# Kernel tuning notes

Measured on AMD Instinct MI355X. Metric: run time of the kernel, lower is better.

## Reference

```python
import jax, jax.numpy as jnp
import numpy as np

H = 16       # num_heads
D = 128      # head dim (TokenShift requires D in {16,32,64,128})
BASE = 10000.0


def _shift_linear(x, W, Ws):
    # ShiftLinear: linear -> (B,T,H,D), then token_shift mixing current token
    # with previous token using data-dependent per-head weights.
    B, T, _ = x.shape
    y = (x @ W.T).reshape(B, T, H, D)
    p = jax.nn.sigmoid(x @ Ws.T)                      # (B,T,H) prev-token weight
    y_prev = jnp.pad(y, ((0, 0), (1, 0), (0, 0), (0, 0)))[:, :T]  # shift right by 1
    return y * (1.0 - p)[..., None] + y_prev * p[..., None]


def _rope(q, k):
    # Non-interleaved half-rotation, signs exactly as in the torch source:
    # y1 = x1*cos + x2*sin ; y2 = -x1*sin + x2*cos
    T = q.shape[1]
    half = D // 2
    inv = 1.0 / (BASE ** (jnp.arange(0, D, 2, dtype=jnp.float32) / D))  # (half,)
    freqs = jnp.outer(jnp.arange(T, dtype=jnp.float32), inv)            # (T,half)
    cos = jnp.cos(freqs)[None, :, None, :]
    sin = jnp.sin(freqs)[None, :, None, :]
    def rot(x):
        x1, x2 = x[..., :half], x[..., half:]
        return jnp.concatenate([x1 * cos + x2 * sin, -x1 * sin + x2 * cos], axis=-1)
    return rot(q), rot(k)


def setup_inputs() -> dict:
    key = jax.random.key(0)
    ks = jax.random.split(key, 10)
    B, T, C = 2, 2048, 2048
    s = 0.02
    return {
        "x":   jax.random.normal(ks[0], (B, T, C), jnp.float32),
        "Wq":  s * jax.random.normal(ks[1], (C, C), jnp.float32),
        "Wsq": s * jax.random.normal(ks[2], (H, C), jnp.float32),
        "Wk":  s * jax.random.normal(ks[3], (C, C), jnp.float32),
        "Wsk": s * jax.random.normal(ks[4], (H, C), jnp.float32),
        "Wv":  s * jax.random.normal(ks[5], (C, C), jnp.float32),
        "Wsv": s * jax.random.normal(ks[6], (H, C), jnp.float32),
        "Wf":  s * jax.random.normal(ks[7], (H, C), jnp.float32),
        "bf":  s * jax.random.normal(ks[8], (H,), jnp.float32),
        "Wo":  s * jax.random.normal(ks[9], (C, C), jnp.float32),
    }


def reference(x, Wq, Wsq, Wk, Wsk, Wv, Wsv, Wf, bf, Wo):
    B, T, C = x.shape
    q = _shift_linear(x, Wq, Wsq)          # (B,T,H,D)
    k = _shift_linear(x, Wk, Wsk)
    v = _shift_linear(x, Wv, Wsv)
    q, k = _rope(q, k)

    # forget gate: log f_t per head, cumulative log-decay
    logf = jax.nn.log_sigmoid(x @ Wf.T + bf)       # (B,T,H)
    cum = jnp.cumsum(logf, axis=1).transpose(0, 2, 1)  # (B,H,T)

    s = jnp.einsum('bthd,bshd->bhts', q, k) / np.sqrt(D).astype(np.float32)
    # decay bias D_ij = sum_{l=j+1}^{i} log f_l = cum_i - cum_j
    s = s + cum[:, :, :, None] - cum[:, :, None, :]
    causal = jnp.tril(jnp.ones((T, T), dtype=bool))
    s = jnp.where(causal[None, None], s, -jnp.inf)
    p = jax.nn.softmax(s, axis=-1)                 # (B,H,T,T)

    o = jnp.einsum('bhts,bshd->bthd', p, v).reshape(B, T, C)
    return o @ Wo.T
```

## Files before the change

### kernel.cpp

```cpp
#include <hip/hip_runtime.h>
#include <math.h>


typedef __attribute__((ext_vector_type(8))) short  shortx8;
typedef __attribute__((ext_vector_type(4))) float  floatx4;

#define DEV __device__ __forceinline__

DEV unsigned short f2bf(float f) {
    unsigned int u = __builtin_bit_cast(unsigned int, f);
    u += 0x7FFFu + ((u >> 16) & 1u);
    return (unsigned short)(u >> 16);
}
DEV float bf2f(unsigned short s) {
    unsigned int u = ((unsigned int)s) << 16;
    return __builtin_bit_cast(float, u);
}
DEV void async16(void* lds, const void* g) {
    __builtin_amdgcn_global_load_lds(
        (const __attribute__((address_space(1))) unsigned int*)g,
        (__attribute__((address_space(3))) unsigned int*)lds, 16, 0, 0);
}

__global__ void cvt_bf16(const float* __restrict__ in, unsigned short* __restrict__ out, int n8) {
    int i = blockIdx.x * 256 + threadIdx.x;
    if (i >= n8) return;
    float4 u = ((const float4*)in)[2 * i];
    float4 v = ((const float4*)in)[2 * i + 1];
    shortx8 r;
    r[0] = (short)f2bf(u.x); r[1] = (short)f2bf(u.y); r[2] = (short)f2bf(u.z); r[3] = (short)f2bf(u.w);
    r[4] = (short)f2bf(v.x); r[5] = (short)f2bf(v.y); r[6] = (short)f2bf(v.z); r[7] = (short)f2bf(v.w);
    *(shortx8*)(out + (size_t)i * 8) = r;
}

__global__ void build_wcat(const float* __restrict__ Wsq, const float* __restrict__ Wsk,
                           const float* __restrict__ Wsv, const float* __restrict__ Wf,
                           unsigned short* __restrict__ out) {
    int i = blockIdx.x * 256 + threadIdx.x;
    int c8 = i & 255;
    int row = i >> 8;
    const float* src = nullptr;
    if      (row < 16) src = Wsq + (size_t)row * 2048;
    else if (row < 32) src = Wsk + (size_t)(row - 16) * 2048;
    else if (row < 48) src = Wsv + (size_t)(row - 32) * 2048;
    else if (row < 64) src = Wf  + (size_t)(row - 48) * 2048;
    shortx8 r = (shortx8){0,0,0,0,0,0,0,0};
    if (src) {
#pragma unroll
        for (int q = 0; q < 8; ++q) r[q] = (short)f2bf(src[c8 * 8 + q]);
    }
    *(shortx8*)(out + (size_t)i * 8) = r;
}

template <typename OutT>
__global__ __launch_bounds__(256)
void gemm_bt(const unsigned short* __restrict__ A, const unsigned short* __restrict__ B,
             OutT* __restrict__ C, int M, int N, int K) {
    __shared__ __align__(16) unsigned short As[2][128 * 32];
    __shared__ __align__(16) unsigned short Bs[2][128 * 32];
    const int tid  = threadIdx.x;
    const int lane = tid & 63;
    const int w    = tid >> 6;
    const int m0   = blockIdx.x * 128;
    const int n0   = blockIdx.y * 128;
    const int wr   = (w >> 1) * 64;
    const int wc   = (w & 1) * 64;
    const int l15  = lane & 15, lg = lane >> 4;
    const int nk   = K >> 5;
    const int c0   = w * 64 + lane;

    floatx4 acc[4][4];
#pragma unroll
    for (int i = 0; i < 4; ++i)
#pragma unroll
        for (int j = 0; j < 4; ++j) acc[i][j] = (floatx4){0.f, 0.f, 0.f, 0.f};

#pragma unroll
    for (int t = 0; t < 2; ++t) {
        int c = t * 256 + c0;
        int row = c >> 2, seg = c & 3;
        async16(&As[0][(t * 256 + w * 64) * 8], A + (size_t)(m0 + row) * K + seg * 8);
        async16(&Bs[0][(t * 256 + w * 64) * 8], B + (size_t)(n0 + row) * K + seg * 8);
    }
    int cur = 0;
    for (int kt = 0; kt < nk; ++kt) {
        __syncthreads();
        if (kt + 1 < nk) {
#pragma unroll
            for (int t = 0; t < 2; ++t) {
                int c = t * 256 + c0;
                int row = c >> 2, seg = c & 3;
                async16(&As[cur ^ 1][(t * 256 + w * 64) * 8],
                        A + (size_t)(m0 + row) * K + (kt + 1) * 32 + seg * 8);
                async16(&Bs[cur ^ 1][(t * 256 + w * 64) * 8],
                        B + (size_t)(n0 + row) * K + (kt + 1) * 32 + seg * 8);
            }
        }
        shortx8 af[4], bfr[4];
#pragma unroll
        for (int i = 0; i < 4; ++i) {
            af[i]  = *(const shortx8*)&As[cur][(wr + i * 16 + l15) * 32 + 8 * lg];
            bfr[i] = *(const shortx8*)&Bs[cur][(wc + i * 16 + l15) * 32 + 8 * lg];
        }
#pragma unroll
        for (int i = 0; i < 4; ++i)
#pragma unroll
            for (int j = 0; j < 4; ++j)
                acc[i][j] = __builtin_amdgcn_mfma_f32_16x16x32_bf16(af[i], bfr[j], acc[i][j], 0, 0, 0);
        cur ^= 1;
    }
#pragma unroll
    for (int i = 0; i < 4; ++i)
#pragma unroll
        for (int j = 0; j < 4; ++j)
#pragma unroll
            for (int r = 0; r < 4; ++r) {
                int row = m0 + wr + i * 16 + 4 * lg + r;
                int col = n0 + wc + j * 16 + l15;
                float v = acc[i][j][r];
                if constexpr (sizeof(OutT) == 2) C[(size_t)row * N + col] = (OutT)f2bf(v);
                else                             C[(size_t)row * N + col] = v;
            }
}

__global__ void cumsum_logf(const float* __restrict__ glog, const float* __restrict__ bfv,
                            float* __restrict__ cum) {
    __shared__ float sums[256];
    const int bh = blockIdx.x, b = bh >> 4, h = bh & 15;
    const int tid = threadIdx.x;
    const float bias = bfv[h];
    float v[8];
    float s = 0.f;
#pragma unroll
    for (int i = 0; i < 8; ++i) {
        int t = tid * 8 + i;
        float z = glog[(size_t)(b * 2048 + t) * 128 + 48 + h] + bias;
        float lf = (z >= 0.f) ? -log1pf(__expf(-z)) : (z - log1pf(__expf(z)));
        s += lf;
        v[i] = s;
    }
    sums[tid] = s;
    __syncthreads();
    for (int off = 1; off < 256; off <<= 1) {
        float t = (tid >= off) ? sums[tid - off] : 0.f;
        __syncthreads();
        sums[tid] += t;
        __syncthreads();
    }
    float basep = sums[tid] - s;
#pragma unroll
    for (int i = 0; i < 8; ++i)
        cum[(size_t)bh * 2048 + tid * 8 + i] = basep + v[i];
}

template <bool ROPE>
__global__ void shift_rope(const unsigned short* __restrict__ Y, int ldY, int yoff,
                           const float* __restrict__ glog, int gcol,
                           unsigned short* __restrict__ Out) {
    int gid = blockIdx.x * 256 + threadIdx.x;
    int j = gid & 7;
    int h = (gid >> 3) & 15;
    int t = (gid >> 7) & 2047;
    int b = gid >> 18;
    const unsigned short* yp = Y + (size_t)(b * 2048 + t) * ldY + yoff + h * 128;
    float z  = glog[(size_t)(b * 2048 + t) * 128 + gcol + h];
    float pg = 1.f / (1.f + __expf(-z));
    shortx8 a1 = *(const shortx8*)(yp + j * 8);
    shortx8 a2 = *(const shortx8*)(yp + 64 + j * 8);
    shortx8 b1 = (shortx8){0,0,0,0,0,0,0,0}, b2 = b1;
    if (t > 0) {
        b1 = *(const shortx8*)(yp - ldY + j * 8);
        b2 = *(const shortx8*)(yp - ldY + 64 + j * 8);
    }
    shortx8 o1, o2;
    const float kf = 13.287712379549449f / 64.f;
#pragma unroll
    for (int i = 0; i < 8; ++i) {
        float m1 = bf2f((unsigned short)a1[i]) * (1.f - pg) + bf2f((unsigned short)b1[i]) * pg;
        float m2 = bf2f((unsigned short)a2[i]) * (1.f - pg) + bf2f((unsigned short)b2[i]) * pg;
        float r1, r2;
        if (ROPE) {
            int d = j * 8 + i;
            float inv = exp2f(-(float)d * kf);
            float ang = (float)t * inv;
            float sv, cv;
            sincosf(ang, &sv, &cv);
            r1 =  m1 * cv + m2 * sv;
            r2 = -m1 * sv + m2 * cv;
        } else { r1 = m1; r2 = m2; }
        o1[i] = (short)f2bf(r1);
        o2[i] = (short)f2bf(r2);
    }
    unsigned short* op = Out + (size_t)((b * 16 + h) * 2048 + t) * 128;
    *(shortx8*)(op + j * 8)      = o1;
    *(shortx8*)(op + 64 + j * 8) = o2;
}

__global__ void transpose_v(const unsigned short* __restrict__ V, unsigned short* __restrict__ Vt) {
    __shared__ unsigned short tile[32][33];
    const int bh = blockIdx.z;
    const int t0 = blockIdx.x * 32, d0 = blockIdx.y * 32;
    const int tx = threadIdx.x, ty = threadIdx.y;
#pragma unroll
    for (int i = 0; i < 4; ++i) {
        int row = ty + i * 8;
        tile[row][tx] = V[(size_t)(bh * 2048 + t0 + row) * 128 + d0 + tx];
    }
    __syncthreads();
#pragma unroll
    for (int i = 0; i < 4; ++i) {
        int drow = ty + i * 8;
        Vt[(size_t)(bh * 128 + d0 + drow) * 2048 + t0 + tx] = tile[tx][drow];
    }
}

__global__ __launch_bounds__(512)
void flash_fwd(const unsigned short* __restrict__ Q, const unsigned short* __restrict__ Km,
               const unsigned short* __restrict__ Vt, const float* __restrict__ cum,
               unsigned short* __restrict__ O) {
    __shared__ __align__(16) unsigned short Ks[2][32 * 128];
    __shared__ __align__(16) unsigned short Vs[2][64 * 64];
    __shared__ __align__(16) unsigned short Plds[8][16][40];
    const int tid = threadIdx.x, lane = tid & 63, w = tid >> 6;
    const int l15 = lane & 15, lg = lane >> 4;
    const int bh = blockIdx.y, b = bh >> 4, h = bh & 15;
    const int qx = (blockIdx.x + bh) & 15;
    const int q0 = qx * 128;
    const int qr = q0 + w * 16;
    const size_t base = (size_t)bh * (2048 * 128);
    const float isd = 0.08838834764831845f;
    const int ntiles = 4 * qx + 4;
    const int myn0 = ((qr + 15) >> 5) + 1;
    const int myn = myn0 < ntiles ? myn0 : ntiles;

    const int ik = w * 64 + lane;
    const int kr = ik >> 4, kc = ik & 15;
    const unsigned short* ksrc = Km + base + (size_t)kr * 128 + ((kc ^ (kr & 7)) * 8);
    const int vr = ik >> 3, vc = ik & 7;
    const int vcc = vc ^ (vr & 7);
    const unsigned short* vsrc = Vt + (size_t)(bh * 128 + 2 * vr + (vcc >> 2)) * 2048 + (vcc & 3) * 8;

    const int kx = l15 & 7;
    const int vconst = ((l15 >> 1) * 64) + ((((l15 & 1) * 4 + lg) ^ ((l15 >> 1) & 7)) * 8);

    shortx8 aq[4];
#pragma unroll
    for (int kk = 0; kk < 4; ++kk)
        aq[kk] = *(const shortx8*)(Q + base + (size_t)(qr + l15) * 128 + kk * 32 + 8 * lg);

    float cum_t[4];
#pragma unroll
    for (int r = 0; r < 4; ++r) cum_t[r] = cum[bh * 2048 + qr + 4 * lg + r];

    floatx4 oacc[8];
#pragma unroll
    for (int d = 0; d < 8; ++d) oacc[d] = (floatx4){0.f, 0.f, 0.f, 0.f};
    float m[4]  = {-1e30f, -1e30f, -1e30f, -1e30f};
    float ls[4] = {0.f, 0.f, 0.f, 0.f};

    async16(&Ks[0][ik * 8], ksrc);
    async16(&Vs[0][ik * 8], vsrc);
    __syncthreads();

    int cur = 0;
    for (int kt = 0; kt < ntiles; ++kt) {
        const int s0 = kt * 32;
        if (kt + 1 < ntiles) {
            async16(&Ks[cur ^ 1][ik * 8], ksrc + (size_t)(kt + 1) * 32 * 128);
            async16(&Vs[cur ^ 1][ik * 8], vsrc + (kt + 1) * 32);
        }
        if (kt < myn) {
            floatx4 sacc[2];
            sacc[0] = (floatx4){0.f, 0.f, 0.f, 0.f};
            sacc[1] = (floatx4){0.f, 0.f, 0.f, 0.f};
#pragma unroll
            for (int sf = 0; sf < 2; ++sf)
#pragma unroll
                for (int kk = 0; kk < 4; ++kk) {
                    shortx8 bk = *(const shortx8*)&Ks[cur][(sf * 16 + l15) * 128 + (((kk * 4 + lg) ^ kx) * 8)];
                    sacc[sf] = __builtin_amdgcn_mfma_f32_16x16x32_bf16(aq[kk], bk, sacc[sf], 0, 0, 0);
                }
            float cs[2];
#pragma unroll
            for (int sf = 0; sf < 2; ++sf) cs[sf] = cum[bh * 2048 + s0 + sf * 16 + l15];

            float p[2][4];
            float tmax[4] = {-1e30f, -1e30f, -1e30f, -1e30f};
            const bool maskt = (s0 + 31 > qr);
#pragma unroll
            for (int sf = 0; sf < 2; ++sf)
#pragma unroll
                for (int r = 0; r < 4; ++r) {
                    float sv = sacc[sf][r] * isd + cum_t[r] - cs[sf];
                    if (maskt) {
                        int trow = qr + 4 * lg + r;
                        int scol = s0 + sf * 16 + l15;
                        if (scol > trow) sv = -1e30f;
                    }
                    p[sf][r] = sv;
                    tmax[r] = fmaxf(tmax[r], sv);
                }
#pragma unroll
            for (int r = 0; r < 4; ++r) {
                tmax[r] = fmaxf(tmax[r], __shfl_xor(tmax[r], 1));
                tmax[r] = fmaxf(tmax[r], __shfl_xor(tmax[r], 2));
                tmax[r] = fmaxf(tmax[r], __shfl_xor(tmax[r], 4));
                tmax[r] = fmaxf(tmax[r], __shfl_xor(tmax[r], 8));
            }
            float scl[4];
#pragma unroll
            for (int r = 0; r < 4; ++r) {
                float mn = fmaxf(m[r], tmax[r]);
                scl[r] = __expf(m[r] - mn);
                m[r] = mn;
            }
            float rs[4] = {0.f, 0.f, 0.f, 0.f};
#pragma unroll
            for (int sf = 0; sf < 2; ++sf)
#pragma unroll
                for (int r = 0; r < 4; ++r) {
                    float e = __expf(p[sf][r] - m[r]);
                    p[sf][r] = e;
                    rs[r] += e;
                }
#pragma unroll
            for (int r = 0; r < 4; ++r) {
                rs[r] += __shfl_xor(rs[r], 1);
                rs[r] += __shfl_xor(rs[r], 2);
                rs[r] += __shfl_xor(rs[r], 4);
                rs[r] += __shfl_xor(rs[r], 8);
                ls[r] = ls[r] * scl[r] + rs[r];
            }
#pragma unroll
            for (int d = 0; d < 8; ++d)
#pragma unroll
                for (int r = 0; r < 4; ++r) oacc[d][r] *= scl[r];

#pragma unroll
            for (int sf = 0; sf < 2; ++sf)
#pragma unroll
                for (int r = 0; r < 4; ++r)
                    Plds[w][4 * lg + r][sf * 16 + l15] = f2bf(p[sf][r]);
            shortx8 pa = *(const shortx8*)&Plds[w][l15][8 * lg];
#pragma unroll
            for (int d = 0; d < 8; ++d) {
                shortx8 bv = *(const shortx8*)&Vs[cur][d * 512 + vconst];
                oacc[d] = __builtin_amdgcn_mfma_f32_16x16x32_bf16(pa, bv, oacc[d], 0, 0, 0);
            }
        }
        __syncthreads();
        cur ^= 1;
    }
#pragma unroll
    for (int r = 0; r < 4; ++r) {
        float inv = 1.f / ls[r];
        int trow = qr + 4 * lg + r;
        size_t ob = (size_t)(b * 2048 + trow) * 2048 + h * 128;
#pragma unroll
        for (int d = 0; d < 8; ++d)
            O[ob + d * 16 + l15] = f2bf(oacc[d][r] * inv);
    }
}

extern "C" void kernel_launch(void* const* d_in, const int* in_sizes, int n_in,
                              void* d_out, int out_size, void* d_ws, size_t ws_size,
                              hipStream_t stream) {
    const float* x   = (const float*)d_in[0];
    const float* Wq  = (const float*)d_in[1];
    const float* Wsq = (const float*)d_in[2];
    const float* Wk  = (const float*)d_in[3];
    const float* Wsk = (const float*)d_in[4];
    const float* Wv  = (const float*)d_in[5];
    const float* Wsv = (const float*)d_in[6];
    const float* Wf  = (const float*)d_in[7];
    const float* bfv = (const float*)d_in[8];
    const float* Wo  = (const float*)d_in[9];
    float* out = (float*)d_out;
    char* ws = (char*)d_ws;

    if (ws_size >= 145489920ull) {
        unsigned short* xb    = (unsigned short*)(ws + 0);
        unsigned short* Wb3   = (unsigned short*)(ws + 16777216);
        unsigned short* wcat  = (unsigned short*)(ws + 41943040);
        float*          glog  = (float*)(ws + 42467328);
        float*          cum   = (float*)(ws + 44564480);
        unsigned short* qbuf  = (unsigned short*)(ws + 44826624);
        unsigned short* kbuf  = (unsigned short*)(ws + 61603840);
        unsigned short* vbuf  = (unsigned short*)(ws + 78381056);
        unsigned short* ybuf3 = (unsigned short*)(ws + 95158272);
        unsigned short* vt    = ybuf3;

        cvt_bf16<<<4096, 256, 0, stream>>>(x, xb, 1048576);
        build_wcat<<<128, 256, 0, stream>>>(Wsq, Wsk, Wsv, Wf, wcat);
        gemm_bt<float><<<dim3(32, 1), 256, 0, stream>>>(xb, wcat, glog, 4096, 128, 2048);
        cumsum_logf<<<32, 256, 0, stream>>>(glog, bfv, cum);

        cvt_bf16<<<2048, 256, 0, stream>>>(Wq, Wb3, 524288);
        cvt_bf16<<<2048, 256, 0, stream>>>(Wk, Wb3 + 4194304, 524288);
        cvt_bf16<<<2048, 256, 0, stream>>>(Wv, Wb3 + 8388608, 524288);
        gemm_bt<unsigned short><<<dim3(32, 48), 256, 0, stream>>>(xb, Wb3, ybuf3, 4096, 6144, 2048);

        shift_rope<true><<<2048, 256, 0, stream>>>(ybuf3, 6144, 0, glog, 0, qbuf);
        shift_rope<true><<<2048, 256, 0, stream>>>(ybuf3, 6144, 2048, glog, 16, kbuf);
        shift_rope<false><<<2048, 256, 0, stream>>>(ybuf3, 6144, 4096, glog, 32, vbuf);
        transpose_v<<<dim3(64, 4, 32), dim3(32, 8), 0, stream>>>(vbuf, vt);

        flash_fwd<<<dim3(16, 32), 512, 0, stream>>>(qbuf, kbuf, vt, cum, xb);

        cvt_bf16<<<2048, 256, 0, stream>>>(Wo, Wb3, 524288);
        gemm_bt<float><<<dim3(32, 16), 256, 0, stream>>>(xb, Wb3, out, 4096, 2048, 2048);
    } else {
        unsigned short* xb   = (unsigned short*)(ws + 0);
        unsigned short* Wb   = (unsigned short*)(ws + 16777216);
        unsigned short* wcat = (unsigned short*)(ws + 25165824);
        float*          glog = (float*)(ws + 25690112);
        float*          cum  = (float*)(ws + 27787264);
        unsigned short* ybuf = (unsigned short*)(ws + 28049408);
        unsigned short* qbuf = (unsigned short*)(ws + 44826624);
        unsigned short* kbuf = (unsigned short*)(ws + 61603840);
        unsigned short* vbuf = (unsigned short*)(ws + 78381056);
        unsigned short* vt   = (unsigned short*)(ws + 95158272);

        cvt_bf16<<<4096, 256, 0, stream>>>(x, xb, 1048576);
        build_wcat<<<128, 256, 0, stream>>>(Wsq, Wsk, Wsv, Wf, wcat);
        gemm_bt<float><<<dim3(32, 1), 256, 0, stream>>>(xb, wcat, glog, 4096, 128, 2048);
        cumsum_logf<<<32, 256, 0, stream>>>(glog, bfv, cum);

        cvt_bf16<<<2048, 256, 0, stream>>>(Wq, Wb, 524288);
        gemm_bt<unsigned short><<<dim3(32, 16), 256, 0, stream>>>(xb, Wb, ybuf, 4096, 2048, 2048);
        shift_rope<true><<<2048, 256, 0, stream>>>(ybuf, 2048, 0, glog, 0, qbuf);

        cvt_bf16<<<2048, 256, 0, stream>>>(Wk, Wb, 524288);
        gemm_bt<unsigned short><<<dim3(32, 16), 256, 0, stream>>>(xb, Wb, ybuf, 4096, 2048, 2048);
        shift_rope<true><<<2048, 256, 0, stream>>>(ybuf, 2048, 0, glog, 16, kbuf);

        cvt_bf16<<<2048, 256, 0, stream>>>(Wv, Wb, 524288);
        gemm_bt<unsigned short><<<dim3(32, 16), 256, 0, stream>>>(xb, Wb, ybuf, 4096, 2048, 2048);
        shift_rope<false><<<2048, 256, 0, stream>>>(ybuf, 2048, 0, glog, 32, vbuf);
        transpose_v<<<dim3(64, 4, 32), dim3(32, 8), 0, stream>>>(vbuf, vt);

        flash_fwd<<<dim3(16, 32), 512, 0, stream>>>(qbuf, kbuf, vt, cum, ybuf);

        cvt_bf16<<<2048, 256, 0, stream>>>(Wo, Wb, 524288);
        gemm_bt<float><<<dim3(32, 16), 256, 0, stream>>>(ybuf, Wb, out, 4096, 2048, 2048);
    }
}
```

Measured before the change: 580.4 us.

## Triple-buffer attention K/V loads, stage cum in LDS, lazy softmax rescale, swizzle GEMM blocks

```diff
diff --git a/kernel.cpp b/kernel.cpp
--- a/kernel.cpp
+++ b/kernel.cpp
@@ -61,8 +61,11 @@
     const int tid  = threadIdx.x;
     const int lane = tid & 63;
     const int w    = tid >> 6;
-    const int m0   = blockIdx.x * 128;
-    const int n0   = blockIdx.y * 128;
+    const int nwg  = gridDim.x * gridDim.y;
+    const int bid0 = blockIdx.y * gridDim.x + blockIdx.x;
+    const int bids = (bid0 & 7) * (nwg >> 3) + (bid0 >> 3);
+    const int m0   = (bids % gridDim.x) * 128;
+    const int n0   = (bids / gridDim.x) * 128;
     const int wr   = (w >> 1) * 64;
     const int wc   = (w & 1) * 64;
     const int l15  = lane & 15, lg = lane >> 4;
@@ -218,8 +221,9 @@
 void flash_fwd(const unsigned short* __restrict__ Q, const unsigned short* __restrict__ Km,
                const unsigned short* __restrict__ Vt, const float* __restrict__ cum,
                unsigned short* __restrict__ O) {
-    __shared__ __align__(16) unsigned short Ks[2][32 * 128];
-    __shared__ __align__(16) unsigned short Vs[2][64 * 64];
+    __shared__ __align__(16) unsigned short Ks[3][32 * 128];
+    __shared__ __align__(16) unsigned short Vs[3][64 * 64];
+    __shared__ __align__(16) float          cumLds[2048];
     __shared__ __align__(16) unsigned short Plds[8][16][40];
     const int tid = threadIdx.x, lane = tid & 63, w = tid >> 6;
     const int l15 = lane & 15, lg = lane >> 4;
@@ -247,10 +251,15 @@
 #pragma unroll
     for (int kk = 0; kk < 4; ++kk)
         aq[kk] = *(const shortx8*)(Q + base + (size_t)(qr + l15) * 128 + kk * 32 + 8 * lg);
-
     float cum_t[4];
 #pragma unroll
     for (int r = 0; r < 4; ++r) cum_t[r] = cum[bh * 2048 + qr + 4 * lg + r];
+
+    async16(&cumLds[ik * 4], cum + (size_t)bh * 2048 + ik * 4);
+    async16(&Ks[0][ik * 8], ksrc);
+    async16(&Vs[0][ik * 8], vsrc);
+    async16(&Ks[1][ik * 8], ksrc + 32 * 128);
+    async16(&Vs[1][ik * 8], vsrc + 32);
 
     floatx4 oacc[8];
 #pragma unroll
@@ -258,18 +267,16 @@
     float m[4]  = {-1e30f, -1e30f, -1e30f, -1e30f};
     float ls[4] = {0.f, 0.f, 0.f, 0.f};
 
-    async16(&Ks[0][ik * 8], ksrc);
-    async16(&Vs[0][ik * 8], vsrc);
-    __syncthreads();
-
-    int cur = 0;
+    int bc = 0, bi = 2;
     for (int kt = 0; kt < ntiles; ++kt) {
-        const int s0 = kt * 32;
-        if (kt + 1 < ntiles) {
-            async16(&Ks[cur ^ 1][ik * 8], ksrc + (size_t)(kt + 1) * 32 * 128);
-            async16(&Vs[cur ^ 1][ik * 8], vsrc + (kt + 1) * 32);
+        asm volatile("s_waitcnt vmcnt(2)" ::: "memory");
+        __builtin_amdgcn_s_barrier();
+        if (kt + 2 < ntiles) {
+            async16(&Ks[bi][ik * 8], ksrc + (size_t)(kt + 2) * 32 * 128);
+            async16(&Vs[bi][ik * 8], vsrc + (kt + 2) * 32);
         }
         if (kt < myn) {
+            const int s0 = kt * 32;
             floatx4 sacc[2];
             sacc[0] = (floatx4){0.f, 0.f, 0.f, 0.f};
             sacc[1] = (floatx4){0.f, 0.f, 0.f, 0.f};
@@ -277,12 +284,12 @@
             for (int sf = 0; sf < 2; ++sf)
 #pragma unroll
                 for (int kk = 0; kk < 4; ++kk) {
-                    shortx8 bk = *(const shortx8*)&Ks[cur][(sf * 16 + l15) * 128 + (((kk * 4 + lg) ^ kx) * 8)];
+                    shortx8 bk = *(const shortx8*)&Ks[bc][(sf * 16 + l15) * 128 + (((kk * 4 + lg) ^ kx) * 8)];
                     sacc[sf] = __builtin_amdgcn_mfma_f32_16x16x32_bf16(aq[kk], bk, sacc[sf], 0, 0, 0);
                 }
             float cs[2];
 #pragma unroll
-            for (int sf = 0; sf < 2; ++sf) cs[sf] = cum[bh * 2048 + s0 + sf * 16 + l15];
+            for (int sf = 0; sf < 2; ++sf) cs[sf] = cumLds[s0 + sf * 16 + l15];
 
             float p[2][4];
             float tmax[4] = {-1e30f, -1e30f, -1e30f, -1e30f};
@@ -307,12 +314,23 @@
                 tmax[r] = fmaxf(tmax[r], __shfl_xor(tmax[r], 4));
                 tmax[r] = fmaxf(tmax[r], __shfl_xor(tmax[r], 8));
             }
-            float scl[4];
-#pragma unroll
-            for (int r = 0; r < 4; ++r) {
-                float mn = fmaxf(m[r], tmax[r]);
-                scl[r] = __expf(m[r] - mn);
-                m[r] = mn;
+            float g = tmax[0] - m[0];
+            g = fmaxf(g, tmax[1] - m[1]);
+            g = fmaxf(g, tmax[2] - m[2]);
+            g = fmaxf(g, tmax[3] - m[3]);
+            if (!__all(g <= 8.0f)) {
+                float scl[4];
+#pragma unroll
+                for (int r = 0; r < 4; ++r) {
+                    float mn = fmaxf(m[r], tmax[r]);
+                    scl[r] = __expf(m[r] - mn);
+                    m[r] = mn;
+                    ls[r] *= scl[r];
+                }
+#pragma unroll
+                for (int d = 0; d < 8; ++d)
+#pragma unroll
+                    for (int r = 0; r < 4; ++r) oacc[d][r] *= scl[r];
             }
             float rs[4] = {0.f, 0.f, 0.f, 0.f};
 #pragma unroll
@@ -329,13 +347,8 @@
                 rs[r] += __shfl_xor(rs[r], 2);
                 rs[r] += __shfl_xor(rs[r], 4);
                 rs[r] += __shfl_xor(rs[r], 8);
-                ls[r] = ls[r] * scl[r] + rs[r];
-            }
-#pragma unroll
-            for (int d = 0; d < 8; ++d)
-#pragma unroll
-                for (int r = 0; r < 4; ++r) oacc[d][r] *= scl[r];
-
+                ls[r] += rs[r];
+            }
 #pragma unroll
             for (int sf = 0; sf < 2; ++sf)
 #pragma unroll
@@ -344,12 +357,12 @@
             shortx8 pa = *(const shortx8*)&Plds[w][l15][8 * lg];
 #pragma unroll
             for (int d = 0; d < 8; ++d) {
-                shortx8 bv = *(const shortx8*)&Vs[cur][d * 512 + vconst];
+                shortx8 bv = *(const shortx8*)&Vs[bc][d * 512 + vconst];
                 oacc[d] = __builtin_amdgcn_mfma_f32_16x16x32_bf16(pa, bv, oacc[d], 0, 0, 0);
             }
         }
-        __syncthreads();
-        cur ^= 1;
+        bc = (bc == 2) ? 0 : bc + 1;
+        bi = (bi == 2) ? 0 : bi + 1;
     }
 #pragma unroll
     for (int r = 0; r < 4; ++r) {
```

Measured after the change: 590.5 us. No clear change (+1.8%).
